# Kernel tuning notes

Measured on AMD Instinct MI355X. Metric: run time of the kernel, lower is better.

Reference implementation:

```python
import jax, jax.numpy as jnp
import numpy as np

N_SEGMENTS = 16384
POINTS_PER_SEG = 64
TOTAL_POINTS = N_SEGMENTS * POINTS_PER_SEG  # 1048576
D_FEAT = 128


def setup_inputs() -> dict:
    key = jax.random.key(0)
    data = jax.random.normal(key, (TOTAL_POINTS, D_FEAT), dtype=jnp.float32)
    # variable-length segment sizes; here uniform 64 so cumsum exactly tiles data,
    # but reference() handles any obj_size with sum == TOTAL_POINTS.
    obj_size = jnp.full((N_SEGMENTS,), POINTS_PER_SEG, dtype=jnp.int32)
    return {"data": data, "obj_size": obj_size}


def reference(data, obj_size):
    # Equivalent of: ends = cumsum(pad(obj_size)); stack([mean(data[a:b], 0) ...])
    # Single-pass segment mean instead of per-segment Python loop.
    n_seg = obj_size.shape[0]
    seg_ids = jnp.repeat(jnp.arange(n_seg, dtype=jnp.int32), obj_size,
                         total_repeat_length=data.shape[0])  # [total_points]
    sums = jax.ops.segment_sum(data, seg_ids, num_segments=n_seg)  # [n_seg, d]
    return sums / obj_size[:, None].astype(data.dtype)
```

## Files before the change

### kernel.cpp

```cpp
#include <hip/hip_runtime.h>
#include <hip/hip_bf16.h>


#define D_FEAT 128
#define FEAT_QUADS (D_FEAT / 4)

__global__ __launch_bounds__(1024) void seg_scan_kernel(
    const int* __restrict__ obj_size, int* __restrict__ offsets, int n_seg) {
  __shared__ int smem[1024];
  const int T = 1024;
  const int tid = threadIdx.x;
  const int per = (n_seg + T - 1) / T;
  const int begin = tid * per;
  const int end = (begin + per < n_seg) ? (begin + per) : n_seg;

  int local = 0;
  for (int i = begin; i < end; ++i) local += obj_size[i];
  smem[tid] = local;
  __syncthreads();

  for (int off = 1; off < T; off <<= 1) {
    int v = 0;
    if (tid >= off) v = smem[tid - off];
    __syncthreads();
    if (tid >= off) smem[tid] += v;
    __syncthreads();
  }

  int excl = (tid == 0) ? 0 : smem[tid - 1];
  for (int i = begin; i < end; ++i) {
    offsets[i] = excl;
    excl += obj_size[i];
  }
}

__global__ __launch_bounds__(256) void seg_mean_kernel(
    const float* __restrict__ data, const int* __restrict__ obj_size,
    const int* __restrict__ offsets, float* __restrict__ out, int n_seg) {
  const int seg = blockIdx.x;
  if (seg >= n_seg) return;

  const int start = offsets[seg];
  const int count = obj_size[seg];

  const int tid = threadIdx.x;
  const int lane_f = tid & 31;
  const int rp = tid >> 5;

  const float4* __restrict__ base = (const float4*)data;

  float4 acc = make_float4(0.f, 0.f, 0.f, 0.f);
  for (int r = rp; r < count; r += 8) {
    float4 v = base[(size_t)(start + r) * FEAT_QUADS + lane_f];
    acc.x += v.x; acc.y += v.y; acc.z += v.z; acc.w += v.w;
  }

  __shared__ float4 smem[256];
  smem[tid] = acc;
  __syncthreads();

  for (int s = 4; s >= 1; s >>= 1) {
    if (rp < s) {
      float4 o = smem[tid + s * 32];
      acc.x += o.x; acc.y += o.y; acc.z += o.z; acc.w += o.w;
      smem[tid] = acc;
    }
    __syncthreads();
  }

  if (rp == 0) {
    const float inv = (count > 0) ? (1.0f / (float)count) : 0.0f;
    float4 r = make_float4(acc.x * inv, acc.y * inv, acc.z * inv, acc.w * inv);
    ((float4*)out)[(size_t)seg * FEAT_QUADS + lane_f] = r;
  }
}

extern "C" void kernel_launch(void* const* d_in, const int* in_sizes, int n_in,
                              void* d_out, int out_size, void* d_ws, size_t ws_size,
                              hipStream_t stream) {
  const float* data = (const float*)d_in[0];
  const int* obj_size = (const int*)d_in[1];
  const int n_seg = in_sizes[1];
  float* out = (float*)d_out;
  int* offsets = (int*)d_ws;

  seg_scan_kernel<<<1, 1024, 0, stream>>>(obj_size, offsets, n_seg);
  seg_mean_kernel<<<n_seg, 256, 0, stream>>>(data, obj_size, offsets, out, n_seg);
}
```

Before: 694.7 us.

## Map one wavefront per segment and use shuffle-based scans and reductions

The mean kernel now assigns one 64-lane wavefront per segment, four segments per block, instead of a whole 256-thread block per segment. Each half-wave takes alternate rows, and the two halves are combined with a single xor shuffle, which removes the shared-memory tree and its barriers. Loads and stores are marked nontemporal. The offset scan uses wave shuffles plus a small cross-wave pass in place of the 10-step shared-memory Hillis-Steele scan. The trade-off is fewer loads in flight per segment, since each wave now walks 32 rows serially.

```diff
diff --git a/kernel.cpp b/kernel.cpp
--- a/kernel.cpp
+++ b/kernel.cpp
@@ -5,29 +5,43 @@
 #define D_FEAT 128
 #define FEAT_QUADS (D_FEAT / 4)
 
+typedef float v4f __attribute__((ext_vector_type(4)));
+
 __global__ __launch_bounds__(1024) void seg_scan_kernel(
     const int* __restrict__ obj_size, int* __restrict__ offsets, int n_seg) {
-  __shared__ int smem[1024];
   const int T = 1024;
   const int tid = threadIdx.x;
+  const int lane = tid & 63;
+  const int wid = tid >> 6;
   const int per = (n_seg + T - 1) / T;
   const int begin = tid * per;
   const int end = (begin + per < n_seg) ? (begin + per) : n_seg;
 
   int local = 0;
   for (int i = begin; i < end; ++i) local += obj_size[i];
-  smem[tid] = local;
+
+  int x = local;
+  #pragma unroll
+  for (int off = 1; off < 64; off <<= 1) {
+    int y = __shfl_up(x, off, 64);
+    if (lane >= off) x += y;
+  }
+
+  __shared__ int wsum[16];
+  if (lane == 63) wsum[wid] = x;
+  __syncthreads();
+  if (tid < 16) {
+    int w = wsum[tid];
+    #pragma unroll
+    for (int off = 1; off < 16; off <<= 1) {
+      int y = __shfl_up(w, off, 64);
+      if (tid >= off) w += y;
+    }
+    wsum[tid] = w;
+  }
   __syncthreads();
 
-  for (int off = 1; off < T; off <<= 1) {
-    int v = 0;
-    if (tid >= off) v = smem[tid - off];
-    __syncthreads();
-    if (tid >= off) smem[tid] += v;
-    __syncthreads();
-  }
-
-  int excl = (tid == 0) ? 0 : smem[tid - 1];
+  int excl = (wid > 0 ? wsum[wid - 1] : 0) + (x - local);
   for (int i = begin; i < end; ++i) {
     offsets[i] = excl;
     excl += obj_size[i];
@@ -37,41 +51,37 @@
 __global__ __launch_bounds__(256) void seg_mean_kernel(
     const float* __restrict__ data, const int* __restrict__ obj_size,
     const int* __restrict__ offsets, float* __restrict__ out, int n_seg) {
-  const int seg = blockIdx.x;
+  const int tid = threadIdx.x;
+  const int wid = tid >> 6;
+  const int lane = tid & 63;
+  const int seg = blockIdx.x * 4 + wid;
   if (seg >= n_seg) return;
 
   const int start = offsets[seg];
   const int count = obj_size[seg];
 
-  const int tid = threadIdx.x;
-  const int lane_f = tid & 31;
-  const int rp = tid >> 5;
+  const int lane_f = lane & 31;
+  const int half = lane >> 5;
 
-  const float4* __restrict__ base = (const float4*)data;
+  const v4f* __restrict__ base =
+      (const v4f*)data + (size_t)start * FEAT_QUADS + lane_f;
 
-  float4 acc = make_float4(0.f, 0.f, 0.f, 0.f);
-  for (int r = rp; r < count; r += 8) {
-    float4 v = base[(size_t)(start + r) * FEAT_QUADS + lane_f];
-    acc.x += v.x; acc.y += v.y; acc.z += v.z; acc.w += v.w;
+  v4f acc = (v4f)(0.0f);
+  for (int r = half; r < count; r += 2) {
+    v4f v = __builtin_nontemporal_load(base + (size_t)r * FEAT_QUADS);
+    acc += v;
   }
 
-  __shared__ float4 smem[256];
-  smem[tid] = acc;
-  __syncthreads();
+  acc.x += __shfl_xor(acc.x, 32, 64);
+  acc.y += __shfl_xor(acc.y, 32, 64);
+  acc.z += __shfl_xor(acc.z, 32, 64);
+  acc.w += __shfl_xor(acc.w, 32, 64);
 
-  for (int s = 4; s >= 1; s >>= 1) {
-    if (rp < s) {
-      float4 o = smem[tid + s * 32];
-      acc.x += o.x; acc.y += o.y; acc.z += o.z; acc.w += o.w;
-      smem[tid] = acc;
-    }
-    __syncthreads();
-  }
-
-  if (rp == 0) {
+  if (half == 0) {
     const float inv = (count > 0) ? (1.0f / (float)count) : 0.0f;
-    float4 r = make_float4(acc.x * inv, acc.y * inv, acc.z * inv, acc.w * inv);
-    ((float4*)out)[(size_t)seg * FEAT_QUADS + lane_f] = r;
+    v4f r = acc * inv;
+    v4f* o = (v4f*)out + (size_t)seg * FEAT_QUADS + lane_f;
+    __builtin_nontemporal_store(r, o);
   }
 }
 
@@ -85,5 +95,7 @@
   int* offsets = (int*)d_ws;
 
   seg_scan_kernel<<<1, 1024, 0, stream>>>(obj_size, offsets, n_seg);
-  seg_mean_kernel<<<n_seg, 256, 0, stream>>>(data, obj_size, offsets, out, n_seg);
+  const int blocks = (n_seg + 3) / 4;
+  seg_mean_kernel<<<blocks, 256, 0, stream>>>(data, obj_size, offsets, out,
+                                              n_seg);
 }
```

After: 677.0 us. -2.5%, faster.
